# Performance work log

Hardware: AMD Instinct MI355X
Metric: run time of the kernel (lower is better)

## Reference

```python
import jax, jax.numpy as jnp
import numpy as np

B, T, D, C = 2, 2048, 1024, 10
F = D // 2 + 1  # rfft bins; permutations act on frequency bins (perm_freq=True)


def setup_inputs() -> dict:
    key = jax.random.key(0)
    ks = jax.random.split(key, 6)
    s = 1.0 / np.sqrt(D)
    x = jax.random.normal(ks[0], (B, T, D), jnp.float32)
    Wq = jax.random.normal(ks[1], (D, D), jnp.float32) * s
    Wk = jax.random.normal(ks[2], (D, D), jnp.float32) * s
    Wv = jax.random.normal(ks[3], (D, D), jnp.float32) * s
    Wo = jax.random.normal(ks[4], (D, D), jnp.float32) * s
    # buffer: torch.randn(C, F).argsort(-1) -> random permutations of freq bins
    perms = jnp.argsort(jax.random.normal(ks[5], (C, F)), axis=-1)
    return {"x": x, "Wq": Wq, "Wk": Wk, "Wv": Wv, "Wo": Wo, "perms": perms}


def reference(x, Wq, Wk, Wv, Wo, perms):
    # linear projections (nn.Linear applies x @ W.T)
    q = x @ Wq.T
    k = x @ Wk.T
    v = x @ Wv.T
    # HRR bind/unbind in rfft frequency domain
    fq = jnp.fft.rfft(q, axis=-1)  # (B,T,F) complex
    fk = jnp.fft.rfft(k, axis=-1)
    fv = jnp.fft.rfft(v, axis=-1)
    # gather permuted redundant copies of freq bins: (B,T,C,F) -> (C,B,T,F)
    fkp = jnp.moveaxis(fk[..., perms], 2, 0)
    fqp = jnp.moveaxis(fq[..., perms], 2, 0)
    # causal associative memory: cumulative sum of key*value bindings over time
    kv = jnp.cumsum(fkp * fv[None], axis=-2)  # (C,B,T,F)
    # unbind with query (circular correlation = multiply by conj), mean copies
    r = jnp.mean(kv * jnp.conj(fqp), axis=0)  # (B,T,F)
    values_hat = jnp.fft.irfft(r, n=D, axis=-1)  # (B,T,D)
    return values_hat @ Wo.T
```

## Files before the change

kernel.cpp:

```cpp
#include <hip/hip_runtime.h>
#include <math.h>

#define B_   2
#define T_   2048
#define D_   1024
#define C_   10
#define F_   513
#define NTOK (B_ * T_)
#define LF   3078
#define LFP  3136
#define KP2  1056
#define NCH  128
#define TC   (T_ / NCH)

typedef unsigned short us16;
typedef __attribute__((ext_vector_type(8))) __bf16 bf16x8;
typedef __attribute__((ext_vector_type(4))) float  f32x4;

#define O_XBF    ((size_t)0)
#define O_PREP   ((size_t)8388608)
#define O_WT     (O_PREP)
#define O_WOBF   (O_PREP + 6291456)
#define O_TCS    (O_PREP + 8388608)
#define O_RCAT   (O_PREP)
#define O_SFB    (O_PREP + 10489856)
#define O_MALLB  (O_SFB + 2162688)
#define O_MOUTB  (O_MALLB + 6303744)
#define O_FALL   (O_MOUTB + 2162688)
#define O_SSCAN  (O_FALL + 25690112)

__device__ __forceinline__ us16 f2b(float f) {
    union { float f; unsigned u; } v; v.f = f;
    unsigned r = v.u + 0x7FFFu + ((v.u >> 16) & 1u);
    return (us16)(r >> 16);
}

__device__ __forceinline__ float2 b2f2(unsigned w) {
    union { unsigned u; float f; } a, b;
    a.u = (w & 0xffffu) << 16;
    b.u = w & 0xffff0000u;
    return make_float2(a.f, b.f);
}

__device__ __forceinline__ void gl_lds16(const us16* g, us16* l) {
    __builtin_amdgcn_global_load_lds(
        (const __attribute__((address_space(1))) unsigned*)g,
        (__attribute__((address_space(3))) unsigned*)l, 16, 0, 0);
}

__global__ __launch_bounds__(256)
void hrr_prep(const float* __restrict__ x,  const float* __restrict__ Wq,
              const float* __restrict__ Wk, const float* __restrict__ Wv,
              const float* __restrict__ Wo,
              us16* __restrict__ Xbf, us16* __restrict__ WT,
              us16* __restrict__ WoBf, us16* __restrict__ Tcs,
              us16* __restrict__ Sfb) {
    __shared__ float t[32][33];
    const int bid = blockIdx.x, tid = threadIdx.x;
    if (bid < 4096) {
        int i = bid * 256 + tid;
        float4 v = ((const float4*)x)[i];
        ushort4 o;
        o.x = f2b(v.x); o.y = f2b(v.y); o.z = f2b(v.z); o.w = f2b(v.w);
        ((ushort4*)Xbf)[i] = o;
    } else if (bid < 5120) {
        int i = (bid - 4096) * 256 + tid;
        float4 v = ((const float4*)Wo)[i];
        ushort4 o;
        o.x = f2b(v.x); o.y = f2b(v.y); o.z = f2b(v.z); o.w = f2b(v.w);
        ((ushort4*)WoBf)[i] = o;
    } else if (bid < 8192) {
        const int l  = bid - 5120;
        const int bz = l >> 10, l2 = l & 1023;
        const int bx = (l2 & 31) * 32, by = (l2 >> 5) * 32;
        const float* W = (bz == 0) ? Wq : (bz == 1) ? Wk : Wv;
        us16* O = WT + (size_t)bz * D_ * D_;
        const int tx = tid & 31, ty = tid >> 5;
#pragma unroll
        for (int i = 0; i < 32; i += 8)
            t[ty + i][tx] = W[(size_t)(by + ty + i) * D_ + bx + tx];
        __syncthreads();
#pragma unroll
        for (int i = 0; i < 32; i += 8)
            O[(size_t)(bx + ty + i) * D_ + by + tx] = f2b(t[tx][ty + i]);
    } else if (bid < 12296) {
        int idx = (bid - 8192) * 256 + tid;
        int r = idx >> 10, e = idx & 1023;
        int f = r >> 1;
        float ang = (float)((f * e) & 1023) * 6.135923151542565e-3f;
        float val = (r & 1) ? -__sinf(ang) : __cosf(ang);
        float s = (f == 0 || f == 512) ? (1.0f / 1024.0f) : (2.0f / 1024.0f);
        Tcs[idx] = f2b(val);
        Sfb[idx] = f2b(s * val);
    } else {
        int idx2 = (bid - 12296) * 256 + tid;
        Sfb[1026 * 1024 + idx2] = 0;
    }
}

template <bool OUT_BF16>
__device__ __forceinline__ void gemm_core64(
    const us16* __restrict__ A, const us16* __restrict__ B, void* __restrict__ Cv,
    int M, int N, int K, int lda, int ldb, int ldc, int Ncap,
    int bm, int bn, us16* smem) {
    us16* As = smem;
    us16* Bs = smem + 8192;

    const int tid  = threadIdx.x;
    const int lane = tid & 63;
    const int wave = tid >> 6;
    const int wm = wave * 32;

    const int r0    = tid >> 2;
    const int g_lds = tid & 3;
    const int g_src = g_lds ^ ((r0 >> 1) & 3);
    const int c4    = g_src * 8;

    int rA0 = bm + r0;      if (rA0 >= M) rA0 = M - 1;
    int rA1 = bm + 64 + r0; if (rA1 >= M) rA1 = M - 1;
    int rB0 = bn + r0;      if (rB0 >= N) rB0 = N - 1;
    const us16* pA0 = A + (size_t)rA0 * lda + c4;
    const us16* pA1 = A + (size_t)rA1 * lda + c4;
    const us16* pB0 = B + (size_t)rB0 * ldb + c4;

    f32x4 acc[2][4];
#pragma unroll
    for (int i = 0; i < 2; i++)
#pragma unroll
        for (int j = 0; j < 4; j++) acc[i][j] = (f32x4){0.f, 0.f, 0.f, 0.f};

    const int fr = lane & 15;
    const int gq = ((lane >> 4) ^ ((fr >> 1) & 3)) * 8;

    const int wb = wave * 512;
#define STAGE_TILE(buf, ko)                                  \
    do {                                                     \
        us16* a_ = As + (buf) * 4096 + wb;                   \
        us16* b_ = Bs + (buf) * 2048 + wb;                   \
        gl_lds16(pA0 + (ko), a_);                            \
        gl_lds16(pA1 + (ko), a_ + 2048);                     \
        gl_lds16(pB0 + (ko), b_);                            \
    } while (0)

    STAGE_TILE(0, 0);
    __syncthreads();

    int cur = 0;
    for (int k0 = 0; k0 < K; k0 += 32) {
        const int kn = k0 + 32;
        if (kn < K) STAGE_TILE(cur ^ 1, kn);

        const us16* Ac = As + cur * 4096;
        const us16* Bc = Bs + cur * 2048;
        bf16x8 af[2], bfr[4];
#pragma unroll
        for (int i = 0; i < 2; i++)
            af[i] = *(const bf16x8*)(Ac + (wm + i * 16 + fr) * 32 + gq);
#pragma unroll
        for (int j = 0; j < 4; j++)
            bfr[j] = *(const bf16x8*)(Bc + (j * 16 + fr) * 32 + gq);
#pragma unroll
        for (int i = 0; i < 2; i++)
#pragma unroll
            for (int j = 0; j < 4; j++)
                acc[i][j] = __builtin_amdgcn_mfma_f32_16x16x32_bf16(bfr[j], af[i], acc[i][j], 0, 0, 0);

        __syncthreads();
        cur ^= 1;
    }
#undef STAGE_TILE

    const int cl  = lane & 15;
    const int rq  = (lane >> 4) * 4;
    float* lbuf = (float*)smem;
#pragma unroll
    for (int p = 0; p < 4; ++p) {
        __syncthreads();
        if (wave == p) {
#pragma unroll
            for (int i = 0; i < 2; ++i) {
                const int rl = i * 16 + cl;
#pragma unroll
                for (int j = 0; j < 4; ++j)
                    *(f32x4*)(lbuf + rl * 68 + j * 16 + rq) = acc[i][j];
            }
        }
        __syncthreads();
        const int rbase = bm + p * 32;
        if (OUT_BF16) {
            us16* C = (us16*)Cv;
            const int row = tid >> 3, col = (tid * 8) & 63;
            const int grow = rbase + row, gcol = bn + col;
            if (grow < M && gcol + 8 <= Ncap) {
                const float* s = lbuf + row * 68 + col;
                uint4 o;
                o.x = (unsigned)f2b(s[0]) | ((unsigned)f2b(s[1]) << 16);
                o.y = (unsigned)f2b(s[2]) | ((unsigned)f2b(s[3]) << 16);
                o.z = (unsigned)f2b(s[4]) | ((unsigned)f2b(s[5]) << 16);
                o.w = (unsigned)f2b(s[6]) | ((unsigned)f2b(s[7]) << 16);
                *(uint4*)(C + (size_t)grow * ldc + gcol) = o;
            }
        } else {
            float* C = (float*)Cv;
#pragma unroll
            for (int rr = 0; rr < 2; ++rr) {
                const int idx = rr * 1024 + tid * 4;
                const int row = idx >> 6, col = idx & 63;
                const int grow = rbase + row, gcol = bn + col;
                if (grow < M && gcol + 4 <= Ncap)
                    *(float4*)(C + (size_t)grow * ldc + gcol) =
                        *(const float4*)(lbuf + row * 68 + col);
            }
        }
    }
}

template <bool OUT_BF16>
__global__ __launch_bounds__(256, 4)
void hrr_gemm(const us16* __restrict__ A, const us16* __restrict__ B,
              void* __restrict__ C, int M, int N, int K,
              int lda, int ldb, int ldc, int Ncap, int swz) {
    __shared__ us16 smem[12288];
    int bx = blockIdx.x, by = blockIdx.y;
    if (swz) {
        const int gx = gridDim.x;
        const int id = bx + gx * by;
        const int q = (gx * gridDim.y) >> 3;
        const int nid = (id & 7) * q + (id >> 3);
        bx = nid % gx; by = nid / gx;
    }
    gemm_core64<OUT_BF16>(A, B, C, M, N, K, lda, ldb, ldc, Ncap,
                          by * 128, bx * 64, smem);
}

__global__ __launch_bounds__(256, 4)
void hrr_gemm_builders(const us16* __restrict__ Tcs, const us16* __restrict__ WT,
                       us16* __restrict__ MallB, const us16* __restrict__ WoBf,
                       const us16* __restrict__ Sfb, us16* __restrict__ MoutB) {
    __shared__ us16 smem[12288];
    const int z = blockIdx.z;
    if (z < 3) {
        if (blockIdx.x >= 16) return;
        gemm_core64<true>(Tcs, WT + (size_t)z * D_ * D_,
                          MallB + (size_t)z * 1026 * 1024,
                          1026, 1024, 1024, 1024, 1024, 1024, 1024,
                          blockIdx.y * 128, blockIdx.x * 64, smem);
    } else {
        if (blockIdx.y >= 8) return;
        gemm_core64<true>(WoBf, Sfb, MoutB,
                          1024, KP2, 1024, 1024, 1024, KP2, KP2,
                          blockIdx.y * 128, blockIdx.x * 64, smem);
    }
}

__global__ __launch_bounds__(512, 2)
void hrr_gemm_main(const us16* __restrict__ A, const us16* __restrict__ B,
                   us16* __restrict__ C) {
    __shared__ us16 smem[65536];
    us16* Asb = smem;
    us16* Bsb = smem + 32768;

    const int tid  = threadIdx.x;
    const int lane = tid & 63;
    const int wave = tid >> 6;

    int id = blockIdx.x + 13 * blockIdx.y;
    id = (id & 7) * 26 + (id >> 3);
    const int bx = id % 13, by = id / 13;
    const int bm = by * 256, bn = bx * 256;

    const int srow = tid >> 3;
    const int sgr  = (tid & 7) ^ (srow & 7);
    const us16* gA[4];
    const us16* gB[4];
#pragma unroll
    for (int g = 0; g < 4; ++g) {
        int ra = bm + g * 64 + srow; if (ra > NTOK - 1) ra = NTOK - 1;
        int rb = bn + g * 64 + srow; if (rb > LF - 1)   rb = LF - 1;
        gA[g] = A + (size_t)ra * 1024 + sgr * 8;
        gB[g] = B + (size_t)rb * 1024 + sgr * 8;
    }

    f32x4 acc[8][4];
#pragma unroll
    for (int i = 0; i < 8; i++)
#pragma unroll
        for (int j = 0; j < 4; j++) acc[i][j] = (f32x4){0.f, 0.f, 0.f, 0.f};

    const int wmw = (wave >> 2) * 128;
    const int wnw = (wave & 3) * 64;
    const int fr  = lane & 15;
    const int gr  = lane >> 4;
    const int l7  = lane & 7;

#define STAGE3(buf, ko)                                            \
    do {                                                           \
        us16* a_ = Asb + (buf) * 16384 + wave * 512;               \
        us16* b_ = Bsb + (buf) * 16384 + wave * 512;               \
        gl_lds16(gA[0] + (ko), a_);                                \
        gl_lds16(gA[1] + (ko), a_ + 4096);                         \
        gl_lds16(gA[2] + (ko), a_ + 8192);                         \
        gl_lds16(gA[3] + (ko), a_ + 12288);                        \
        gl_lds16(gB[0] + (ko), b_);                                \
        gl_lds16(gB[1] + (ko), b_ + 4096);                         \
        gl_lds16(gB[2] + (ko), b_ + 8192);                         \
        gl_lds16(gB[3] + (ko), b_ + 12288);                        \
    } while (0)

#define RBAR                                                       \
    do {                                                           \
        asm volatile("" ::: "memory");                             \
        __builtin_amdgcn_s_barrier();                              \
        asm volatile("" ::: "memory");                             \
    } while (0)

#define LOAD_A(ih)                                                              \
    do {                                                                        \
        _Pragma("unroll")                                                       \
        for (int i = 0; i < 4; ++i)                                             \
            _Pragma("unroll")                                                   \
            for (int ks = 0; ks < 2; ++ks)                                      \
                af[i][ks] = *(const bf16x8*)(Ac +                               \
                    (wmw + (ih) * 64 + i * 16 + fr) * 64 +                      \
                    (((ks << 2) | gr) ^ l7) * 8);                               \
    } while (0)

#define LOAD_B(jh)                                                              \
    do {                                                                        \
        _Pragma("unroll")                                                       \
        for (int j = 0; j < 2; ++j)                                             \
            _Pragma("unroll")                                                   \
            for (int ks = 0; ks < 2; ++ks)                                      \
                bfr[j][ks] = *(const bf16x8*)(Bc +                              \
                    (wnw + (jh) * 32 + j * 16 + fr) * 64 +                      \
                    (((ks << 2) | gr) ^ l7) * 8);                               \
    } while (0)

#define MFMA_Q(ih, jh)                                                          \
    do {                                                                        \
        __builtin_amdgcn_s_setprio(1);                                          \
        _Pragma("unroll")                                                       \
        for (int i = 0; i < 4; ++i)                                             \
            _Pragma("unroll")                                                   \
            for (int j = 0; j < 2; ++j)                                         \
                _Pragma("unroll")                                               \
                for (int ks = 0; ks < 2; ++ks)                                  \
                    acc[(ih) * 4 + i][(jh) * 2 + j] =                           \
                        __builtin_amdgcn_mfma_f32_16x16x32_bf16(                \
                            bfr[j][ks], af[i][ks],                              \
                            acc[(ih) * 4 + i][(jh) * 2 + j], 0, 0, 0);          \
        __builtin_amdgcn_s_setprio(0);                                          \
    } while (0)

    STAGE3(0, 0);
    asm volatile("s_waitcnt vmcnt(0)" ::: "memory");
    __builtin_amdgcn_s_barrier();
    asm volatile("" ::: "memory");

    int cur = 0;
#pragma unroll 1
    for (int t = 0; t < 16; ++t) {
        if (t < 15) STAGE3(cur ^ 1, (t + 1) * 64);

        const us16* Ac = Asb + cur * 16384;
        const us16* Bc = Bsb + cur * 16384;
        bf16x8 af[4][2], bfr[2][2];

        LOAD_A(0); LOAD_B(0); MFMA_Q(0, 0); RBAR;
        LOAD_B(1);            MFMA_Q(0, 1); RBAR;
        LOAD_A(1);            MFMA_Q(1, 1); RBAR;
        LOAD_B(0);            MFMA_Q(1, 0);
        asm volatile("s_waitcnt vmcnt(0)" ::: "memory");
        __builtin_amdgcn_s_barrier();
        asm volatile("" ::: "memory");
        cur ^= 1;
    }
#undef STAGE3
#undef LOAD_A
#undef LOAD_B
#undef MFMA_Q
#undef RBAR

    __syncthreads();
    float* lw = (float*)smem + wave * (32 * 68);
    const int cl = lane & 15;
    const int rq = (lane >> 4) * 4;
#pragma unroll
    for (int p = 0; p < 4; ++p) {
#pragma unroll
        for (int ii = 0; ii < 2; ++ii) {
            const int ifr = p * 2 + ii;
#pragma unroll
            for (int j = 0; j < 4; ++j)
                *(f32x4*)(lw + (ii * 16 + cl) * 68 + j * 16 + rq) = acc[ifr][j];
        }
        __syncthreads();
#pragma unroll
        for (int rr = 0; rr < 4; ++rr) {
            const int idx = rr * 512 + lane * 8;
            const int row = idx >> 6, col = idx & 63;
            const int grow = bm + wmw + p * 32 + row;
            const int gcol = bn + wnw + col;
            if (gcol + 8 <= LFP) {
                const float* s = lw + row * 68 + col;
                uint4 o;
                o.x = (unsigned)f2b(s[0]) | ((unsigned)f2b(s[1]) << 16);
                o.y = (unsigned)f2b(s[2]) | ((unsigned)f2b(s[3]) << 16);
                o.z = (unsigned)f2b(s[4]) | ((unsigned)f2b(s[5]) << 16);
                o.w = (unsigned)f2b(s[6]) | ((unsigned)f2b(s[7]) << 16);
                *(uint4*)(C + (size_t)grow * LFP + gcol) = o;
            }
        }
        __syncthreads();
    }
}

__global__ __launch_bounds__(512, 4)
void hrr_scan_sums(const us16* __restrict__ Fall, const int* __restrict__ perms,
                   float* __restrict__ S) {
    const int n = blockIdx.x, b = blockIdx.y;
    const int tid = threadIdx.x;
    __shared__ float2 kc[F_], vc[F_];

    float aR[2][C_], aI[2][C_];
    int gg[2][C_];
#pragma unroll
    for (int i = 0; i < 2; i++) {
        const int f = (i == 0) ? tid : 512;
        const bool act = (i == 0) || (tid == 0);
#pragma unroll
        for (int c = 0; c < C_; c++) {
            gg[i][c] = act ? perms[c * F_ + f] : 0;
            aR[i][c] = aI[i][c] = 0.f;
        }
    }

    const unsigned* rowb =
        (const unsigned*)(Fall + (size_t)(b * T_ + n * TC) * LFP);
    const int R32 = LFP / 2;

    unsigned rk0, rk2 = 0, rv0, rv1 = 0;
#define SFETCH(tl)                                                   \
    do {                                                             \
        const unsigned* r_ = rowb + (size_t)(tl) * R32;              \
        rk0 = r_[513 + tid];                                         \
        rv0 = r_[1026 + tid];                                        \
        if (tid == 0) { rk2 = r_[1025]; rv1 = r_[1538]; }            \
    } while (0)

    SFETCH(0);
    for (int tl = 0; tl < TC; tl++) {
        __syncthreads();
        kc[tid] = b2f2(rk0);
        vc[tid] = b2f2(rv0);
        if (tid == 0) { kc[512] = b2f2(rk2); vc[512] = b2f2(rv1); }
        __syncthreads();
        if (tl + 1 < TC) SFETCH(tl + 1);
#pragma unroll
        for (int i = 0; i < 2; i++) {
            const int lv = (i == 0) ? tid : 512;
            if (i == 0 || tid == 0) {
                float2 v = vc[lv];
#pragma unroll
                for (int c = 0; c < C_; c++) {
                    float2 k = kc[gg[i][c]];
                    aR[i][c] += k.x * v.x - k.y * v.y;
                    aI[i][c] += k.x * v.y + k.y * v.x;
                }
            }
        }
    }
#undef SFETCH
#pragma unroll
    for (int i = 0; i < 2; i++) {
        const int f = (i == 0) ? tid : 512;
        if (i == 0 || tid == 0) {
#pragma unroll
            for (int c = 0; c < C_; c++) {
                size_t a = ((((size_t)c * B_ + b) * NCH + n) * F_ + f) * 2;
                S[a] = aR[i][c]; S[a + 1] = aI[i][c];
            }
        }
    }
}

__global__ void hrr_scan_prefix(float* __restrict__ S) {
    int tid = blockIdx.x * 256 + threadIdx.x;
    if (tid >= C_ * B_ * F_) return;
    int c = tid / (B_ * F_);
    int r = tid % (B_ * F_);
    int b = r / F_, f = r % F_;
    size_t base = (((size_t)c * B_ + b) * NCH) * F_ + f;
    float runR = 0.f, runI = 0.f;
    for (int n0 = 0; n0 < NCH; n0 += 8) {
        float tR[8], tI[8];
#pragma unroll
        for (int u = 0; u < 8; u++) {
            size_t a = (base + (size_t)(n0 + u) * F_) * 2;
            tR[u] = S[a]; tI[u] = S[a + 1];
        }
#pragma unroll
        for (int u = 0; u < 8; u++) {
            size_t a = (base + (size_t)(n0 + u) * F_) * 2;
            S[a] = runR; S[a + 1] = runI;
            runR += tR[u]; runI += tI[u];
        }
    }
}

__global__ __launch_bounds__(512, 4)
void hrr_scan_apply(const us16* __restrict__ Fall, const int* __restrict__ perms,
                    const float* __restrict__ S, us16* __restrict__ Rcat) {
    const int n = blockIdx.x, b = blockIdx.y;
    const int tid = threadIdx.x;
    __shared__ float2 qc[F_], kc[F_], vc[F_];

    float kvR[2][C_], kvI[2][C_];
    int gg[2][C_];
#pragma unroll
    for (int i = 0; i < 2; i++) {
        const int f = (i == 0) ? tid : 512;
        const bool act = (i == 0) || (tid == 0);
#pragma unroll
        for (int c = 0; c < C_; c++) {
            gg[i][c] = act ? perms[c * F_ + f] : 0;
            if (act) {
                size_t a = ((((size_t)c * B_ + b) * NCH + n) * F_ + f) * 2;
                kvR[i][c] = S[a]; kvI[i][c] = S[a + 1];
            } else { kvR[i][c] = 0.f; kvI[i][c] = 0.f; }
        }
    }

    const unsigned* rowb =
        (const unsigned*)(Fall + (size_t)(b * T_ + n * TC) * LFP);
    const int R32 = LFP / 2;

    unsigned rq0, rq2 = 0, rk0, rk2 = 0, rv0, rv1 = 0;
#define AFETCH(tl)                                                   \
    do {                                                             \
        const unsigned* r_ = rowb + (size_t)(tl) * R32;              \
        rq0 = r_[tid];                                               \
        rk0 = r_[513 + tid];                                         \
        rv0 = r_[1026 + tid];                                        \
        if (tid == 0) { rq2 = r_[512]; rk2 = r_[1025]; rv1 = r_[1538]; } \
    } while (0)

    AFETCH(0);
    for (int tl = 0; tl < TC; tl++) {
        const int tt = b * T_ + n * TC + tl;
        __syncthreads();
        qc[tid] = b2f2(rq0);
        kc[tid] = b2f2(rk0);
        vc[tid] = b2f2(rv0);
        if (tid == 0) {
            qc[512] = b2f2(rq2); kc[512] = b2f2(rk2); vc[512] = b2f2(rv1);
        }
        __syncthreads();
        if (tl + 1 < TC) AFETCH(tl + 1);
        unsigned* out32 = (unsigned*)(Rcat + (size_t)tt * KP2);
#pragma unroll
        for (int i = 0; i < 2; i++) {
            const int f = (i == 0) ? tid : 512;
            const int lv = (i == 0) ? tid : 512;
            if (i == 0 || tid == 0) {
                float2 v = vc[lv];
                float accR = 0.f, accI = 0.f;
#pragma unroll
                for (int c = 0; c < C_; c++) {
                    int g = gg[i][c];
                    float2 k = kc[g];
                    float nR = kvR[i][c] + k.x * v.x - k.y * v.y;
                    float nI = kvI[i][c] + k.x * v.y + k.y * v.x;
                    kvR[i][c] = nR; kvI[i][c] = nI;
                    float2 q = qc[g];
                    accR += nR * q.x + nI * q.y;
                    accI += nI * q.x - nR * q.y;
                }
                out32[f] = (unsigned)f2b(accR * 0.1f)
                         | ((unsigned)f2b(accI * 0.1f) << 16);
            }
        }
        if (tid < 15)
            out32[513 + tid] = 0;
    }
#undef AFETCH
}

extern "C" void kernel_launch(void* const* d_in, const int* in_sizes, int n_in,
                              void* d_out, int out_size, void* d_ws, size_t ws_size,
                              hipStream_t stream) {
    const float* x  = (const float*)d_in[0];
    const float* Wq = (const float*)d_in[1];
    const float* Wk = (const float*)d_in[2];
    const float* Wv = (const float*)d_in[3];
    const float* Wo = (const float*)d_in[4];
    const int* perms = (const int*)d_in[5];
    float* out = (float*)d_out;

    char* ws = (char*)d_ws;
    us16* Xbf   = (us16*)(ws + O_XBF);
    us16* WT    = (us16*)(ws + O_WT);
    us16* WoBf  = (us16*)(ws + O_WOBF);
    us16* Tcs   = (us16*)(ws + O_TCS);
    us16* Sfb   = (us16*)(ws + O_SFB);
    us16* MallB = (us16*)(ws + O_MALLB);
    us16* MoutB = (us16*)(ws + O_MOUTB);
    us16* Rcat  = (us16*)(ws + O_RCAT);
    us16* Fall  = (us16*)(ws + O_FALL);
    float* Ssc  = (float*)(ws + O_SSCAN);

    hrr_prep<<<12416, 256, 0, stream>>>(x, Wq, Wk, Wv, Wo, Xbf, WT, WoBf, Tcs, Sfb);

    hrr_gemm_builders<<<dim3(17, 9, 4), 256, 0, stream>>>(Tcs, WT, MallB, WoBf, Sfb, MoutB);

    hrr_gemm_main<<<dim3(13, 16), 512, 0, stream>>>(Xbf, MallB, Fall);

    hrr_scan_sums<<<dim3(NCH, B_), 512, 0, stream>>>(Fall, perms, Ssc);
    hrr_scan_prefix<<<(C_ * B_ * F_ + 255) / 256, 256, 0, stream>>>(Ssc);
    hrr_scan_apply<<<dim3(NCH, B_), 512, 0, stream>>>(Fall, perms, Ssc, Rcat);

    hrr_gemm<false><<<dim3(16, 32), 256, 0, stream>>>(
        Rcat, MoutB, out, NTOK, D_, KP2, KP2, KP2, D_, D_, 1);
}
```

Baseline: 215.2 us.

## Fuse three scan kernels into one persistent kernel with grid barriers

Merges the chunk-sum, prefix and apply scan kernels into one kernel of 256 blocks. Two atomic-counter grid-wide barriers replace the kernel boundaries, and the counters are reset in the prep kernel. This removes two launches and their inter-kernel gaps. It relies on all 256 blocks being co-resident, which is why launch bounds drop to 2 blocks per SM, and the spin-waiting adds synchronisation cost.

```diff
diff --git a/kernel.cpp b/kernel.cpp
--- a/kernel.cpp
+++ b/kernel.cpp
@@ -12,6 +12,7 @@
 #define KP2  1056
 #define NCH  128
 #define TC   (T_ / NCH)
+#define NSCB (NCH * B_)
 
 typedef unsigned short us16;
 typedef __attribute__((ext_vector_type(8))) __bf16 bf16x8;
@@ -28,6 +29,7 @@
 #define O_MOUTB  (O_MALLB + 6303744)
 #define O_FALL   (O_MOUTB + 2162688)
 #define O_SSCAN  (O_FALL + 25690112)
+#define O_CTR    (O_SSCAN + 10506240)
 
 __device__ __forceinline__ us16 f2b(float f) {
     union { float f; unsigned u; } v; v.f = f;
@@ -54,7 +56,7 @@
               const float* __restrict__ Wo,
               us16* __restrict__ Xbf, us16* __restrict__ WT,
               us16* __restrict__ WoBf, us16* __restrict__ Tcs,
-              us16* __restrict__ Sfb) {
+              us16* __restrict__ Sfb, unsigned* __restrict__ ctr) {
     __shared__ float t[32][33];
     const int bid = blockIdx.x, tid = threadIdx.x;
     if (bid < 4096) {
@@ -95,6 +97,7 @@
     } else {
         int idx2 = (bid - 12296) * 256 + tid;
         Sfb[1026 * 1024 + idx2] = 0;
+        if (bid == 12296 && tid < 2) ctr[tid] = 0;
     }
 }
 
@@ -415,175 +418,185 @@
     }
 }
 
-__global__ __launch_bounds__(512, 4)
-void hrr_scan_sums(const us16* __restrict__ Fall, const int* __restrict__ perms,
-                   float* __restrict__ S) {
+__global__ __launch_bounds__(512, 2)
+void hrr_scan_fused(const us16* __restrict__ Fall, const int* __restrict__ perms,
+                    float* __restrict__ S, us16* __restrict__ Rcat,
+                    unsigned* __restrict__ ctr) {
     const int n = blockIdx.x, b = blockIdx.y;
     const int tid = threadIdx.x;
-    __shared__ float2 kc[F_], vc[F_];
-
-    float aR[2][C_], aI[2][C_];
-    int gg[2][C_];
-#pragma unroll
-    for (int i = 0; i < 2; i++) {
-        const int f = (i == 0) ? tid : 512;
-        const bool act = (i == 0) || (tid == 0);
-#pragma unroll
-        for (int c = 0; c < C_; c++) {
-            gg[i][c] = act ? perms[c * F_ + f] : 0;
-            aR[i][c] = aI[i][c] = 0.f;
-        }
-    }
+    __shared__ float2 qc[F_], kc[F_], vc[F_];
 
     const unsigned* rowb =
         (const unsigned*)(Fall + (size_t)(b * T_ + n * TC) * LFP);
     const int R32 = LFP / 2;
 
-    unsigned rk0, rk2 = 0, rv0, rv1 = 0;
-#define SFETCH(tl)                                                   \
-    do {                                                             \
-        const unsigned* r_ = rowb + (size_t)(tl) * R32;              \
-        rk0 = r_[513 + tid];                                         \
-        rv0 = r_[1026 + tid];                                        \
-        if (tid == 0) { rk2 = r_[1025]; rv1 = r_[1538]; }            \
-    } while (0)
-
-    SFETCH(0);
-    for (int tl = 0; tl < TC; tl++) {
-        __syncthreads();
-        kc[tid] = b2f2(rk0);
-        vc[tid] = b2f2(rv0);
-        if (tid == 0) { kc[512] = b2f2(rk2); vc[512] = b2f2(rv1); }
-        __syncthreads();
-        if (tl + 1 < TC) SFETCH(tl + 1);
-#pragma unroll
-        for (int i = 0; i < 2; i++) {
-            const int lv = (i == 0) ? tid : 512;
-            if (i == 0 || tid == 0) {
-                float2 v = vc[lv];
-#pragma unroll
-                for (int c = 0; c < C_; c++) {
-                    float2 k = kc[gg[i][c]];
-                    aR[i][c] += k.x * v.x - k.y * v.y;
-                    aI[i][c] += k.x * v.y + k.y * v.x;
-                }
-            }
-        }
-    }
-#undef SFETCH
-#pragma unroll
-    for (int i = 0; i < 2; i++) {
-        const int f = (i == 0) ? tid : 512;
-        if (i == 0 || tid == 0) {
-#pragma unroll
-            for (int c = 0; c < C_; c++) {
-                size_t a = ((((size_t)c * B_ + b) * NCH + n) * F_ + f) * 2;
-                S[a] = aR[i][c]; S[a + 1] = aI[i][c];
-            }
-        }
-    }
-}
-
-__global__ void hrr_scan_prefix(float* __restrict__ S) {
-    int tid = blockIdx.x * 256 + threadIdx.x;
-    if (tid >= C_ * B_ * F_) return;
-    int c = tid / (B_ * F_);
-    int r = tid % (B_ * F_);
-    int b = r / F_, f = r % F_;
-    size_t base = (((size_t)c * B_ + b) * NCH) * F_ + f;
-    float runR = 0.f, runI = 0.f;
-    for (int n0 = 0; n0 < NCH; n0 += 8) {
-        float tR[8], tI[8];
-#pragma unroll
-        for (int u = 0; u < 8; u++) {
-            size_t a = (base + (size_t)(n0 + u) * F_) * 2;
-            tR[u] = S[a]; tI[u] = S[a + 1];
-        }
-#pragma unroll
-        for (int u = 0; u < 8; u++) {
-            size_t a = (base + (size_t)(n0 + u) * F_) * 2;
-            S[a] = runR; S[a + 1] = runI;
-            runR += tR[u]; runI += tI[u];
-        }
-    }
-}
-
-__global__ __launch_bounds__(512, 4)
-void hrr_scan_apply(const us16* __restrict__ Fall, const int* __restrict__ perms,
-                    const float* __restrict__ S, us16* __restrict__ Rcat) {
-    const int n = blockIdx.x, b = blockIdx.y;
-    const int tid = threadIdx.x;
-    __shared__ float2 qc[F_], kc[F_], vc[F_];
-
-    float kvR[2][C_], kvI[2][C_];
-    int gg[2][C_];
-#pragma unroll
-    for (int i = 0; i < 2; i++) {
-        const int f = (i == 0) ? tid : 512;
-        const bool act = (i == 0) || (tid == 0);
-#pragma unroll
-        for (int c = 0; c < C_; c++) {
-            gg[i][c] = act ? perms[c * F_ + f] : 0;
-            if (act) {
-                size_t a = ((((size_t)c * B_ + b) * NCH + n) * F_ + f) * 2;
-                kvR[i][c] = S[a]; kvI[i][c] = S[a + 1];
-            } else { kvR[i][c] = 0.f; kvI[i][c] = 0.f; }
-        }
-    }
-
-    const unsigned* rowb =
-        (const unsigned*)(Fall + (size_t)(b * T_ + n * TC) * LFP);
-    const int R32 = LFP / 2;
-
-    unsigned rq0, rq2 = 0, rk0, rk2 = 0, rv0, rv1 = 0;
-#define AFETCH(tl)                                                   \
-    do {                                                             \
-        const unsigned* r_ = rowb + (size_t)(tl) * R32;              \
-        rq0 = r_[tid];                                               \
-        rk0 = r_[513 + tid];                                         \
-        rv0 = r_[1026 + tid];                                        \
-        if (tid == 0) { rq2 = r_[512]; rk2 = r_[1025]; rv1 = r_[1538]; } \
-    } while (0)
-
-    AFETCH(0);
-    for (int tl = 0; tl < TC; tl++) {
-        const int tt = b * T_ + n * TC + tl;
-        __syncthreads();
-        qc[tid] = b2f2(rq0);
-        kc[tid] = b2f2(rk0);
-        vc[tid] = b2f2(rv0);
-        if (tid == 0) {
-            qc[512] = b2f2(rq2); kc[512] = b2f2(rk2); vc[512] = b2f2(rv1);
-        }
-        __syncthreads();
-        if (tl + 1 < TC) AFETCH(tl + 1);
-        unsigned* out32 = (unsigned*)(Rcat + (size_t)tt * KP2);
+    {
+        float aR[2][C_], aI[2][C_];
+        int gg[2][C_];
 #pragma unroll
         for (int i = 0; i < 2; i++) {
             const int f = (i == 0) ? tid : 512;
-            const int lv = (i == 0) ? tid : 512;
+            const bool act = (i == 0) || (tid == 0);
+#pragma unroll
+            for (int c = 0; c < C_; c++) {
+                gg[i][c] = act ? perms[c * F_ + f] : 0;
+                aR[i][c] = aI[i][c] = 0.f;
+            }
+        }
+        unsigned rk0, rk2 = 0, rv0, rv1 = 0;
+#define SFETCH(tl)                                                   \
+        do {                                                         \
+            const unsigned* r_ = rowb + (size_t)(tl) * R32;          \
+            rk0 = r_[513 + tid];                                     \
+            rv0 = r_[1026 + tid];                                    \
+            if (tid == 0) { rk2 = r_[1025]; rv1 = r_[1538]; }        \
+        } while (0)
+        SFETCH(0);
+        for (int tl = 0; tl < TC; tl++) {
+            __syncthreads();
+            kc[tid] = b2f2(rk0);
+            vc[tid] = b2f2(rv0);
+            if (tid == 0) { kc[512] = b2f2(rk2); vc[512] = b2f2(rv1); }
+            __syncthreads();
+            if (tl + 1 < TC) SFETCH(tl + 1);
+#pragma unroll
+            for (int i = 0; i < 2; i++) {
+                const int lv = (i == 0) ? tid : 512;
+                if (i == 0 || tid == 0) {
+                    float2 v = vc[lv];
+#pragma unroll
+                    for (int c = 0; c < C_; c++) {
+                        float2 k = kc[gg[i][c]];
+                        aR[i][c] += k.x * v.x - k.y * v.y;
+                        aI[i][c] += k.x * v.y + k.y * v.x;
+                    }
+                }
+            }
+        }
+#undef SFETCH
+#pragma unroll
+        for (int i = 0; i < 2; i++) {
+            const int f = (i == 0) ? tid : 512;
             if (i == 0 || tid == 0) {
-                float2 v = vc[lv];
-                float accR = 0.f, accI = 0.f;
 #pragma unroll
                 for (int c = 0; c < C_; c++) {
-                    int g = gg[i][c];
-                    float2 k = kc[g];
-                    float nR = kvR[i][c] + k.x * v.x - k.y * v.y;
-                    float nI = kvI[i][c] + k.x * v.y + k.y * v.x;
-                    kvR[i][c] = nR; kvI[i][c] = nI;
-                    float2 q = qc[g];
-                    accR += nR * q.x + nI * q.y;
-                    accI += nI * q.x - nR * q.y;
+                    size_t a = ((((size_t)c * B_ + b) * NCH + n) * F_ + f) * 2;
+                    S[a] = aR[i][c]; S[a + 1] = aI[i][c];
                 }
-                out32[f] = (unsigned)f2b(accR * 0.1f)
-                         | ((unsigned)f2b(accI * 0.1f) << 16);
-            }
-        }
-        if (tid < 15)
-            out32[513 + tid] = 0;
-    }
+            }
+        }
+    }
+
+    __threadfence();
+    __syncthreads();
+    if (tid == 0) {
+        atomicAdd(&ctr[0], 1u);
+        while (atomicAdd(&ctr[0], 0u) < (unsigned)NSCB)
+            __builtin_amdgcn_s_sleep(2);
+    }
+    __syncthreads();
+    __threadfence();
+
+    {
+        int gid = (b * NCH + n) * 512 + tid;
+        if (gid < C_ * B_ * F_) {
+            int c = gid / (B_ * F_);
+            int r = gid % (B_ * F_);
+            int bb = r / F_, f = r % F_;
+            size_t base = (((size_t)c * B_ + bb) * NCH) * F_ + f;
+            float runR = 0.f, runI = 0.f;
+            for (int n0 = 0; n0 < NCH; n0 += 8) {
+                float tR[8], tI[8];
+#pragma unroll
+                for (int u = 0; u < 8; u++) {
+                    size_t a = (base + (size_t)(n0 + u) * F_) * 2;
+                    tR[u] = S[a]; tI[u] = S[a + 1];
+                }
+#pragma unroll
+                for (int u = 0; u < 8; u++) {
+                    size_t a = (base + (size_t)(n0 + u) * F_) * 2;
+                    S[a] = runR; S[a + 1] = runI;
+                    runR += tR[u]; runI += tI[u];
+                }
+            }
+        }
+    }
+
+    __threadfence();
+    __syncthreads();
+    if (tid == 0) {
+        atomicAdd(&ctr[1], 1u);
+        while (atomicAdd(&ctr[1], 0u) < (unsigned)NSCB)
+            __builtin_amdgcn_s_sleep(2);
+    }
+    __syncthreads();
+    __threadfence();
+
+    {
+        float kvR[2][C_], kvI[2][C_];
+        int gg[2][C_];
+#pragma unroll
+        for (int i = 0; i < 2; i++) {
+            const int f = (i == 0) ? tid : 512;
+            const bool act = (i == 0) || (tid == 0);
+#pragma unroll
+            for (int c = 0; c < C_; c++) {
+                gg[i][c] = act ? perms[c * F_ + f] : 0;
+                if (act) {
+                    size_t a = ((((size_t)c * B_ + b) * NCH + n) * F_ + f) * 2;
+                    kvR[i][c] = S[a]; kvI[i][c] = S[a + 1];
+                } else { kvR[i][c] = 0.f; kvI[i][c] = 0.f; }
+            }
+        }
+        unsigned rq0, rq2 = 0, rk0, rk2 = 0, rv0, rv1 = 0;
+#define AFETCH(tl)                                                   \
+        do {                                                         \
+            const unsigned* r_ = rowb + (size_t)(tl) * R32;          \
+            rq0 = r_[tid];                                           \
+            rk0 = r_[513 + tid];                                     \
+            rv0 = r_[1026 + tid];                                    \
+            if (tid == 0) { rq2 = r_[512]; rk2 = r_[1025]; rv1 = r_[1538]; } \
+        } while (0)
+        AFETCH(0);
+        for (int tl = 0; tl < TC; tl++) {
+            const int tt = b * T_ + n * TC + tl;
+            __syncthreads();
+            qc[tid] = b2f2(rq0);
+            kc[tid] = b2f2(rk0);
+            vc[tid] = b2f2(rv0);
+            if (tid == 0) {
+                qc[512] = b2f2(rq2); kc[512] = b2f2(rk2); vc[512] = b2f2(rv1);
+            }
+            __syncthreads();
+            if (tl + 1 < TC) AFETCH(tl + 1);
+            unsigned* out32 = (unsigned*)(Rcat + (size_t)tt * KP2);
+#pragma unroll
+            for (int i = 0; i < 2; i++) {
+                const int f = (i == 0) ? tid : 512;
+                const int lv = (i == 0) ? tid : 512;
+                if (i == 0 || tid == 0) {
+                    float2 v = vc[lv];
+                    float accR = 0.f, accI = 0.f;
+#pragma unroll
+                    for (int c = 0; c < C_; c++) {
+                        int g = gg[i][c];
+                        float2 k = kc[g];
+                        float nR = kvR[i][c] + k.x * v.x - k.y * v.y;
+                        float nI = kvI[i][c] + k.x * v.y + k.y * v.x;
+                        kvR[i][c] = nR; kvI[i][c] = nI;
+                        float2 q = qc[g];
+                        accR += nR * q.x + nI * q.y;
+                        accI += nI * q.x - nR * q.y;
+                    }
+                    out32[f] = (unsigned)f2b(accR * 0.1f)
+                             | ((unsigned)f2b(accI * 0.1f) << 16);
+                }
+            }
+            if (tid < 15)
+                out32[513 + tid] = 0;
+        }
 #undef AFETCH
+    }
 }
 
 extern "C" void kernel_launch(void* const* d_in, const int* in_sizes, int n_in,
@@ -608,16 +621,15 @@
     us16* Rcat  = (us16*)(ws + O_RCAT);
     us16* Fall  = (us16*)(ws + O_FALL);
     float* Ssc  = (float*)(ws + O_SSCAN);
-
-    hrr_prep<<<12416, 256, 0, stream>>>(x, Wq, Wk, Wv, Wo, Xbf, WT, WoBf, Tcs, Sfb);
+    unsigned* ctr = (unsigned*)(ws + O_CTR);
+
+    hrr_prep<<<12416, 256, 0, stream>>>(x, Wq, Wk, Wv, Wo, Xbf, WT, WoBf, Tcs, Sfb, ctr);
 
     hrr_gemm_builders<<<dim3(17, 9, 4), 256, 0, stream>>>(Tcs, WT, MallB, WoBf, Sfb, MoutB);
 
     hrr_gemm_main<<<dim3(13, 16), 512, 0, stream>>>(Xbf, MallB, Fall);
 
-    hrr_scan_sums<<<dim3(NCH, B_), 512, 0, stream>>>(Fall, perms, Ssc);
-    hrr_scan_prefix<<<(C_ * B_ * F_ + 255) / 256, 256, 0, stream>>>(Ssc);
-    hrr_scan_apply<<<dim3(NCH, B_), 512, 0, stream>>>(Fall, perms, Ssc, Rcat);
+    hrr_scan_fused<<<dim3(NCH, B_), 512, 0, stream>>>(Fall, perms, Ssc, Rcat, ctr);
 
     hrr_gemm<false><<<dim3(16, 32), 256, 0, stream>>>(
         Rcat, MoutB, out, NTOK, D_, KP2, KP2, KP2, D_, D_, 1);
```

Measured after the change: 412.8 us. +91.8%, slower.
